# Kernel tuning notes

Hardware: AMD Instinct MI355X
Metric: run time of the kernel (lower is better)

Reference implementation:

```python
import jax, jax.numpy as jnp
import numpy as np

HIDDEN = 1024
N_HEADS = 16
HEAD_DIM = HIDDEN // N_HEADS


def setup_inputs() -> dict:
    key = jax.random.key(0)
    ks = jax.random.split(key, 7)
    b, l, m = 4, 1024, 1024
    q = jax.random.normal(ks[0], (b, l, HIDDEN), dtype=jnp.float32)
    k = jax.random.normal(ks[1], (b, m, HIDDEN), dtype=jnp.float32)
    v = jax.random.normal(ks[2], (b, m, HIDDEN), dtype=jnp.float32)
    s = 1.0 / np.sqrt(HIDDEN)
    w_q = jax.random.normal(ks[3], (HIDDEN, HIDDEN), dtype=jnp.float32) * s
    w_k = jax.random.normal(ks[4], (HIDDEN, HIDDEN), dtype=jnp.float32) * s
    w_v = jax.random.normal(ks[5], (HIDDEN, HIDDEN), dtype=jnp.float32) * s
    w_o = jax.random.normal(ks[6], (HIDDEN, HIDDEN), dtype=jnp.float32) * s
    return {"q": q, "k": k, "v": v, "w_q": w_q, "w_k": w_k, "w_v": w_v, "w_o": w_o}


def reference(q, k, v, w_q, w_k, w_v, w_o):
    b, l, _ = q.shape
    _, m, _ = k.shape
    # Linear (bias=False): y = x @ W^T
    qp = q @ w_q.T
    kp = k @ w_k.T
    vp = v @ w_v.T  # projected but unused downstream (faithful to original bug)
    # Faithful non-standard split: hidden -> (head_dim, n_heads)
    qh = qp.reshape(b, l, HEAD_DIM, N_HEADS)
    kh = kp.reshape(b, m, HEAD_DIM, N_HEADS)
    # attn over K, scaled, softmax over m (dim=2)
    scores = jnp.einsum('bldn,bmdn->blmn', qh, kh) / np.sqrt(HEAD_DIM)
    attn = jax.nn.softmax(scores, axis=2)
    # dropout is identity in eval mode
    # NOTE: original attends over K (not V) — reproduced faithfully
    x = jnp.einsum('blmn,bmdn->bldn', attn, kh)
    x = x.reshape(b, l, HIDDEN)  # 'b l d n -> b l (d n)'
    return x @ w_o.T
```

## Files before the change

kernel.cpp:

```cpp
#include <hip/hip_runtime.h>
#include <hip/hip_bf16.h>
#include <stdint.h>
#include <math.h>


typedef __bf16 bf16;
typedef __bf16 bf16x8 __attribute__((ext_vector_type(8)));
typedef __bf16 bf16x4 __attribute__((ext_vector_type(4)));
typedef float  f32x4  __attribute__((ext_vector_type(4)));
typedef float  f32x16 __attribute__((ext_vector_type(16)));

__device__ __forceinline__ void async_load16(const void* g, void* l) {
  __builtin_amdgcn_global_load_lds((__attribute__((address_space(1))) void*)g,
                                   (__attribute__((address_space(3))) void*)l,
                                   16, 0, 0);
}

__device__ __forceinline__ void join_pin() {
  __builtin_amdgcn_sched_barrier(0);
  __builtin_amdgcn_s_barrier();
  __builtin_amdgcn_sched_barrier(0);
}

__device__ __forceinline__ int detect_fl(const void* samp, int tid, int* smax) {
  int e = (((const unsigned short*)samp)[tid] >> 7) & 0xFF;
#pragma unroll
  for (int off = 1; off <= 32; off <<= 1) {
    int o = __shfl_xor(e, off);
    e = o > e ? o : e;
  }
  if ((tid & 63) == 0) smax[tid >> 6] = e;
  __syncthreads();
  int m01 = smax[0] > smax[1] ? smax[0] : smax[1];
  int m23 = smax[2] > smax[3] ? smax[2] : smax[3];
  return ((m01 > m23 ? m01 : m23) >= 140) ? 1 : 0;
}

__global__ void __launch_bounds__(256)
canon(const void* __restrict__ q, const void* __restrict__ k,
      const void* __restrict__ wq, const void* __restrict__ wk,
      const void* __restrict__ wo,
      bf16* __restrict__ qc, bf16* __restrict__ kc,
      bf16* __restrict__ wqc, bf16* __restrict__ wkc,
      bf16* __restrict__ wo_p, int* __restrict__ flag) {
  __shared__ int smax[4];
  const int tid = threadIdx.x;
  const int fl = detect_fl(q, tid, smax);
  if (blockIdx.x == 0 && tid == 0) *flag = fl;

  const size_t e0 = (size_t)blockIdx.x * 2048 + tid * 8;
  const size_t M4 = 4194304, M8 = 8388608, M9 = 9437184, M10 = 10485760;
  const void* src; bf16* dst; size_t le; bool perm = false;
  if (e0 < M4)       { src = q;  dst = qc;   le = e0;       }
  else if (e0 < M8)  { src = k;  dst = kc;   le = e0 - M4;  }
  else if (e0 < M9)  { src = wq; dst = wqc;  le = e0 - M8;  }
  else if (e0 < M10) { src = wk; dst = wkc;  le = e0 - M9;  }
  else               { src = wo; dst = wo_p; le = e0 - M10; perm = true; }

  if (!perm) {
    bf16x8 v;
    if (fl) {
      const float* p = (const float*)src + le;
      f32x4 a = *(const f32x4*)p, b = *(const f32x4*)(p + 4);
#pragma unroll
      for (int j = 0; j < 4; ++j) { v[j] = (bf16)a[j]; v[4 + j] = (bf16)b[j]; }
    } else {
      v = *(const bf16x8*)((const bf16*)src + le);
    }
    *(bf16x8*)(dst + le) = v;
  } else {
    int o = (int)(le >> 10), kp0 = (int)(le & 1023);
    bf16x8 v;
#pragma unroll
    for (int j = 0; j < 8; ++j) {
      int kp = kp0 + j;
      int h = ((kp & 63) << 4) | (kp >> 6);
      float f = fl ? ((const float*)src)[o * 1024 + h]
                   : (float)((const bf16*)src)[o * 1024 + h];
      f = fminf(fmaxf(f, -1024.f), 1024.f);
      v[j] = (bf16)f;
    }
    *(bf16x8*)(dst + le) = v;
  }
}

__global__ void __launch_bounds__(256, 3)
qk_gemm(const bf16* __restrict__ qc, const bf16* __restrict__ wqc,
        const bf16* __restrict__ kc, const bf16* __restrict__ wkc,
        bf16* __restrict__ qh, bf16* __restrict__ kh, bf16* __restrict__ khT,
        float cs) {
  __shared__ __align__(16) char smem[49152];
  bf16* const sA0 = (bf16*)smem;
  bf16* const sA1 = (bf16*)(smem + 16384);
  bf16* const sB0 = (bf16*)(smem + 32768);
  bf16* const sB1 = (bf16*)(smem + 40960);
  bf16* const epi = (bf16*)smem;

  const int tid  = threadIdx.x;
  const int lane = tid & 63;
  const int wave = tid >> 6;
  const int q4   = lane >> 4;
  const int c16  = lane & 15;
  const int wm   = wave >> 1;
  const int wn   = wave & 1;

  const int z = blockIdx.z;
  const bf16* A = z ? kc : qc;
  const bf16* W = z ? wkc : wqc;
  const float scale = z ? 1.0f : cs;
  bf16* out0 = z ? kh : qh;

  const int lin    = blockIdx.x + 8 * blockIdx.y;
  const int rowBlk = (lin & 31) * 128;
  const int colBlk = (lin >> 5) * 64;

  const bf16* gA[4]; int lA[4];
#pragma unroll
  for (int i = 0; i < 4; ++i) {
    int s = tid + 256 * i;
    int r = s >> 3, g = (s & 7) ^ (r & 7);
    gA[i] = A + (size_t)(rowBlk + r) * 1024 + g * 8;
    lA[i] = s * 8;
  }
  const bf16* gB[2]; int lB[2];
#pragma unroll
  for (int i = 0; i < 2; ++i) {
    int s = tid + 256 * i;
    int r = s >> 3, g = (s & 7) ^ (r & 7);
    gB[i] = W + (size_t)(colBlk + r) * 1024 + g * 8;
    lB[i] = s * 8;
  }

  f32x4 acc[4][2] = {};

#pragma unroll
  for (int i = 0; i < 4; ++i) async_load16(gA[i], sA0 + lA[i]);
#pragma unroll
  for (int i = 0; i < 2; ++i) async_load16(gB[i], sB0 + lB[i]);

  for (int t = 0; t < 16; ++t) {
    if (t < 15) {
      const int kn = (t + 1) * 64;
      bf16* dA = (t & 1) ? sA0 : sA1;
      bf16* dB = (t & 1) ? sB0 : sB1;
#pragma unroll
      for (int i = 0; i < 4; ++i) async_load16(gA[i] + kn, dA + lA[i]);
#pragma unroll
      for (int i = 0; i < 2; ++i) async_load16(gB[i] + kn, dB + lB[i]);
      asm volatile("s_waitcnt vmcnt(6)" ::: "memory");
    } else {
      asm volatile("s_waitcnt vmcnt(0)" ::: "memory");
    }
    join_pin();

    const bf16* cA = (t & 1) ? sA1 : sA0;
    const bf16* cB = (t & 1) ? sB1 : sB0;
#pragma unroll
    for (int ks = 0; ks < 2; ++ks) {
      bf16x8 af[4], bfr[2];
#pragma unroll
      for (int mt = 0; mt < 4; ++mt) {
        int row = wm * 64 + mt * 16 + c16;
        af[mt] = *(const bf16x8*)(cA + row * 64 +
                   (((ks * 4 + q4) ^ (row & 7)) * 8));
      }
#pragma unroll
      for (int nt = 0; nt < 2; ++nt) {
        int row = wn * 32 + nt * 16 + c16;
        bfr[nt] = *(const bf16x8*)(cB + row * 64 +
                   (((ks * 4 + q4) ^ (row & 7)) * 8));
      }
#pragma unroll
      for (int mt = 0; mt < 4; ++mt)
#pragma unroll
        for (int nt = 0; nt < 2; ++nt)
          acc[mt][nt] = __builtin_amdgcn_mfma_f32_16x16x32_bf16(
              af[mt], bfr[nt], acc[mt][nt], 0, 0, 0);
    }
    asm volatile("s_waitcnt lgkmcnt(0)" ::: "memory");
    join_pin();
  }

#pragma unroll
  for (int mt = 0; mt < 4; ++mt)
#pragma unroll
    for (int nt = 0; nt < 2; ++nt)
#pragma unroll
      for (int r = 0; r < 4; ++r) {
        int m_t = wm * 64 + mt * 16 + q4 * 4 + r;
        int c   = wn * 32 + nt * 16 + c16;
        epi[m_t * 70 + c] = (bf16)(acc[mt][nt][r] * scale);
      }
  __syncthreads();

  const int bb    = rowBlk >> 10;
  const int mbase = rowBlk & 1023;
  const int dg0   = colBlk >> 4;

  {
    int n = tid >> 4;
#pragma unroll
    for (int i = 0; i < 8; ++i) {
      int m_t = (tid & 15) + i * 16;
      bf16x4 v;
#pragma unroll
      for (int dt = 0; dt < 4; ++dt) v[dt] = epi[m_t * 70 + dt * 16 + n];
      *(bf16x4*)(out0 + ((size_t)(bb * 16 + n) * 1024 + mbase + m_t) * 64 + dg0) = v;
    }
  }
  if (z) {
    int r = tid >> 2, qtr = tid & 3;
    int n = r >> 2, dt = r & 3;
    int c = dt * 16 + n;
    size_t base = ((size_t)(bb * 16 + n) * 64 + dg0 + dt) * 1024 + mbase + qtr * 32;
#pragma unroll
    for (int c8 = 0; c8 < 4; ++c8) {
      bf16x8 v;
#pragma unroll
      for (int j = 0; j < 8; ++j) v[j] = epi[(qtr * 32 + c8 * 8 + j) * 70 + c];
      *(bf16x8*)(khT + base + c8 * 8) = v;
    }
  }
}

__global__ void __launch_bounds__(256, 2)
attn_kernel(const bf16* __restrict__ qh, const bf16* __restrict__ kh,
            const bf16* __restrict__ khT, bf16* __restrict__ xh) {
  __shared__ __align__(16) bf16 sK[2][64 * 64];
  __shared__ __align__(16) bf16 sKT[2][64 * 64];
  __shared__ __align__(16) bf16 sP[4][32 * 72];

  const int tid  = threadIdx.x;
  const int lane = tid & 63;
  const int wave = tid >> 6;
  const int n32  = lane & 31;
  const int hk   = lane >> 5;
  const int lin  = blockIdx.x;
  const int bn   = lin & 63;
  const int qt   = lin >> 6;
  const int b    = bn >> 4, n = bn & 15;
  const int l0w  = qt * 128 + wave * 32;

  const bf16* qhead  = qh  + (size_t)bn * (1024 * 64);
  const bf16* khead  = kh  + (size_t)bn * (1024 * 64);
  const bf16* kThead = khT + (size_t)bn * (64 * 1024);

  bf16x8 aq[4];
#pragma unroll
  for (int kc = 0; kc < 4; ++kc)
    aq[kc] = *(const bf16x8*)(qhead + (size_t)(l0w + n32) * 64 + kc * 16 + hk * 8);

  int kr[2], kg[2];
#pragma unroll
  for (int i = 0; i < 2; ++i) {
    int s = tid + 256 * i;
    kr[i] = s >> 3;  kg[i] = (s & 7) ^ (kr[i] & 7);
  }

  f32x16 O[2] = {};
  f32x16 Osum = {};
  bf16x8 ones;
#pragma unroll
  for (int j = 0; j < 8; ++j) ones[j] = (bf16)1.0f;
  bf16* sPw = sP[wave];

#pragma unroll
  for (int i = 0; i < 2; ++i) {
    int s = (tid + 256 * i) * 8;
    async_load16(khead + (size_t)kr[i] * 64 + kg[i] * 8, &sK[0][s]);
    async_load16(kThead + (size_t)kr[i] * 1024 + kg[i] * 8, &sKT[0][s]);
  }

  for (int t = 0; t < 16; ++t) {
    if (t < 15) {
      const int m0n = (t + 1) * 64;
      const int bi  = (t + 1) & 1;
#pragma unroll
      for (int i = 0; i < 2; ++i) {
        int s = (tid + 256 * i) * 8;
        async_load16(khead + (size_t)(m0n + kr[i]) * 64 + kg[i] * 8, &sK[bi][s]);
        async_load16(kThead + (size_t)kr[i] * 1024 + m0n + kg[i] * 8, &sKT[bi][s]);
      }
      asm volatile("s_waitcnt vmcnt(4)" ::: "memory");
    } else {
      asm volatile("s_waitcnt vmcnt(0)" ::: "memory");
    }
    join_pin();

    const bf16* cK  = sK[t & 1];
    const bf16* cKT = sKT[t & 1];

    f32x16 S0 = {}, S1 = {};
    __builtin_amdgcn_s_setprio(1);
#pragma unroll
    for (int kc = 0; kc < 4; ++kc) {
      int G = kc * 2 + hk;
      int R0 = n32, R1 = 32 + n32;
      bf16x8 bk0 = *(const bf16x8*)(cK + R0 * 64 + ((G ^ (R0 & 7)) * 8));
      bf16x8 bk1 = *(const bf16x8*)(cK + R1 * 64 + ((G ^ (R1 & 7)) * 8));
      S0 = __builtin_amdgcn_mfma_f32_32x32x16_bf16(aq[kc], bk0, S0, 0, 0, 0);
      S1 = __builtin_amdgcn_mfma_f32_32x32x16_bf16(aq[kc], bk1, S1, 0, 0, 0);
    }
    __builtin_amdgcn_s_setprio(0);

#pragma unroll
    for (int r = 0; r < 16; ++r) {
      int qrow = (r & 3) + 8 * (r >> 2) + 4 * hk;
      sPw[qrow * 72 + n32]      = (bf16)__builtin_amdgcn_exp2f(S0[r]);
      sPw[qrow * 72 + 32 + n32] = (bf16)__builtin_amdgcn_exp2f(S1[r]);
    }

    bf16x8 ap[4];
    __builtin_amdgcn_s_setprio(1);
#pragma unroll
    for (int kc = 0; kc < 4; ++kc) {
      ap[kc] = *(const bf16x8*)(sPw + n32 * 72 + kc * 16 + hk * 8);
      Osum = __builtin_amdgcn_mfma_f32_32x32x16_bf16(ap[kc], ones, Osum, 0, 0, 0);
    }
#pragma unroll
    for (int dt = 0; dt < 2; ++dt) {
#pragma unroll
      for (int kc = 0; kc < 4; ++kc) {
        int R = dt * 32 + n32;
        int G = kc * 2 + hk;
        bf16x8 bkt = *(const bf16x8*)(cKT + R * 64 + ((G ^ (R & 7)) * 8));
        O[dt] = __builtin_amdgcn_mfma_f32_32x32x16_bf16(ap[kc], bkt, O[dt], 0, 0, 0);
      }
    }
    __builtin_amdgcn_s_setprio(0);
    asm volatile("s_waitcnt lgkmcnt(0)" ::: "memory");
    join_pin();
  }

  {
    float inv[16];
#pragma unroll
    for (int r = 0; r < 16; ++r) inv[r] = 1.0f / Osum[r];
#pragma unroll
    for (int dt = 0; dt < 2; ++dt)
#pragma unroll
      for (int r = 0; r < 16; ++r) {
        int qrow = (r & 3) + 8 * (r >> 2) + 4 * hk;
        sPw[qrow * 72 + dt * 32 + n32] = (bf16)(O[dt][r] * inv[r]);
      }
  }
  {
    int l_loc = lane >> 1, dh = lane & 1;
    size_t base = ((size_t)(b * 1024 + l0w + l_loc) * 16 + n) * 64 + dh * 32;
#pragma unroll
    for (int c8 = 0; c8 < 4; ++c8) {
      bf16x8 v = *(const bf16x8*)(sPw + l_loc * 72 + dh * 32 + c8 * 8);
      *(bf16x8*)(xh + base + c8 * 8) = v;
    }
  }
}

__global__ void __launch_bounds__(256, 4)
o_gemm(const bf16* __restrict__ A, const bf16* __restrict__ W,
       bf16* __restrict__ out0, float* __restrict__ outf,
       const int* __restrict__ flag) {
  __shared__ __align__(16) bf16 sA[2][64 * 64];
  __shared__ __align__(16) bf16 sB[2][64 * 64];

  const int tid  = threadIdx.x;
  const int lane = tid & 63;
  const int wave = tid >> 6;
  const int q4   = lane >> 4;
  const int c16  = lane & 15;
  const int wm   = wave >> 1;
  const int wn   = wave & 1;

  const int lin    = blockIdx.x + 8 * blockIdx.y;
  const int rowBlk = (lin & 63) * 64;
  const int colBlk = (lin >> 6) * 64;

  const bf16* gA[2]; const bf16* gB[2]; int ls[2];
#pragma unroll
  for (int i = 0; i < 2; ++i) {
    int s = tid + 256 * i;
    int r = s >> 3, g = (s & 7) ^ (r & 7);
    gA[i] = A + (size_t)(rowBlk + r) * 1024 + g * 8;
    gB[i] = W + (size_t)(colBlk + r) * 1024 + g * 8;
    ls[i] = s * 8;
  }

  f32x4 acc[2][2] = {};

#pragma unroll
  for (int i = 0; i < 2; ++i) {
    async_load16(gA[i], &sA[0][ls[i]]);
    async_load16(gB[i], &sB[0][ls[i]]);
  }

  for (int t = 0; t < 16; ++t) {
    if (t < 15) {
      const int kn = (t + 1) * 64;
      const int bi = (t + 1) & 1;
#pragma unroll
      for (int i = 0; i < 2; ++i) {
        async_load16(gA[i] + kn, &sA[bi][ls[i]]);
        async_load16(gB[i] + kn, &sB[bi][ls[i]]);
      }
      asm volatile("s_waitcnt vmcnt(4)" ::: "memory");
    } else {
      asm volatile("s_waitcnt vmcnt(0)" ::: "memory");
    }
    join_pin();

    const bf16* cA = sA[t & 1];
    const bf16* cB = sB[t & 1];
#pragma unroll
    for (int ks = 0; ks < 2; ++ks) {
      bf16x8 af[2], bfr[2];
#pragma unroll
      for (int mt = 0; mt < 2; ++mt) {
        int row = wm * 32 + mt * 16 + c16;
        af[mt] = *(const bf16x8*)(cA + row * 64 +
                   (((ks * 4 + q4) ^ (row & 7)) * 8));
      }
#pragma unroll
      for (int nt = 0; nt < 2; ++nt) {
        int row = wn * 32 + nt * 16 + c16;
        bfr[nt] = *(const bf16x8*)(cB + row * 64 +
                   (((ks * 4 + q4) ^ (row & 7)) * 8));
      }
#pragma unroll
      for (int mt = 0; mt < 2; ++mt)
#pragma unroll
        for (int nt = 0; nt < 2; ++nt)
          acc[mt][nt] = __builtin_amdgcn_mfma_f32_16x16x32_bf16(
              af[mt], bfr[nt], acc[mt][nt], 0, 0, 0);
    }
    asm volatile("s_waitcnt lgkmcnt(0)" ::: "memory");
    join_pin();
  }

  const int fl = *flag;
#pragma unroll
  for (int mt = 0; mt < 2; ++mt)
#pragma unroll
    for (int nt = 0; nt < 2; ++nt)
#pragma unroll
      for (int r = 0; r < 4; ++r) {
        int gm = rowBlk + wm * 32 + mt * 16 + q4 * 4 + r;
        int gn = colBlk + wn * 32 + nt * 16 + c16;
        size_t idx = (size_t)gm * 1024 + gn;
        if (fl) outf[idx] = acc[mt][nt][r];
        else    out0[idx] = (bf16)acc[mt][nt][r];
      }
}

extern "C" void kernel_launch(void* const* d_in, const int* in_sizes, int n_in,
                              void* d_out, int out_size, void* d_ws, size_t ws_size,
                              hipStream_t stream) {
  const void* q_raw  = d_in[0];
  const void* k_raw  = d_in[1];
  const void* wq_raw = d_in[3];
  const void* wk_raw = d_in[4];
  const void* wo_raw = d_in[6];

  char* ws = (char*)d_ws;
  const size_t MB = 1024 * 1024;
  bf16* qc   = (bf16*)(ws + 0 * MB);
  bf16* kc   = (bf16*)(ws + 8 * MB);
  bf16* kh   = (bf16*)(ws + 16 * MB);
  bf16* wqc  = (bf16*)(ws + 24 * MB);
  bf16* wkc  = (bf16*)(ws + 26 * MB);
  bf16* wo_p = (bf16*)(ws + 28 * MB);
  int*  flag = (int*)(ws + 30 * MB);
  bf16* xh   = qc;
  bf16* qh   = (bf16*)d_out;
  bf16* khT  = (bf16*)((char*)d_out + 8 * MB);

  const float CS = 0.125f * 1.4426950408889634f;
  dim3 blk(256, 1, 1);

  hipLaunchKernelGGL(canon, dim3(5632), blk, 0, stream,
                     q_raw, k_raw, wq_raw, wk_raw, wo_raw,
                     qc, kc, wqc, wkc, wo_p, flag);
  hipLaunchKernelGGL(qk_gemm, dim3(8, 64, 2), blk, 0, stream,
                     qc, wqc, kc, wkc, qh, kh, khT, CS);
  hipLaunchKernelGGL(attn_kernel, dim3(512), blk, 0, stream,
                     qh, kh, khT, xh);
  hipLaunchKernelGGL(o_gemm, dim3(8, 128), blk, 0, stream,
                     xh, wo_p, (bf16*)d_out, (float*)d_out, flag);
}
```

Before: 188.3 us.

## Fuse fp32-to-bf16 activation conversion into the QK projection GEMM loads

The q and k activations are no longer converted to bf16 in a separate pass. The QK GEMM now reads the raw fp32 (or bf16) activations into registers, converts them, and stores them to LDS, prefetching one tile ahead. The canon kernel now handles only the weights. This removes a full read-and-write round trip of 8M activation elements and shrinks the canon launch. In exchange, the GEMM A-side loses its async direct-to-LDS loads, does twice the global bytes per tile in fp32 mode, and adds register pressure, conversion ALU work and an extra LDS wait.

```diff
diff --git a/kernel.cpp b/kernel.cpp
--- a/kernel.cpp
+++ b/kernel.cpp
@@ -37,10 +37,8 @@
 }
 
 __global__ void __launch_bounds__(256)
-canon(const void* __restrict__ q, const void* __restrict__ k,
-      const void* __restrict__ wq, const void* __restrict__ wk,
-      const void* __restrict__ wo,
-      bf16* __restrict__ qc, bf16* __restrict__ kc,
+canon(const void* __restrict__ q, const void* __restrict__ wq,
+      const void* __restrict__ wk, const void* __restrict__ wo,
       bf16* __restrict__ wqc, bf16* __restrict__ wkc,
       bf16* __restrict__ wo_p, int* __restrict__ flag) {
   __shared__ int smax[4];
@@ -49,13 +47,11 @@
   if (blockIdx.x == 0 && tid == 0) *flag = fl;
 
   const size_t e0 = (size_t)blockIdx.x * 2048 + tid * 8;
-  const size_t M4 = 4194304, M8 = 8388608, M9 = 9437184, M10 = 10485760;
+  const size_t M1 = 1048576, M2 = 2097152;
   const void* src; bf16* dst; size_t le; bool perm = false;
-  if (e0 < M4)       { src = q;  dst = qc;   le = e0;       }
-  else if (e0 < M8)  { src = k;  dst = kc;   le = e0 - M4;  }
-  else if (e0 < M9)  { src = wq; dst = wqc;  le = e0 - M8;  }
-  else if (e0 < M10) { src = wk; dst = wkc;  le = e0 - M9;  }
-  else               { src = wo; dst = wo_p; le = e0 - M10; perm = true; }
+  if (e0 < M1)      { src = wq; dst = wqc;  le = e0;      }
+  else if (e0 < M2) { src = wk; dst = wkc;  le = e0 - M1; }
+  else              { src = wo; dst = wo_p; le = e0 - M2; perm = true; }
 
   if (!perm) {
     bf16x8 v;
@@ -85,8 +81,8 @@
 }
 
 __global__ void __launch_bounds__(256, 3)
-qk_gemm(const bf16* __restrict__ qc, const bf16* __restrict__ wqc,
-        const bf16* __restrict__ kc, const bf16* __restrict__ wkc,
+qk_gemm(const void* __restrict__ q_raw, const bf16* __restrict__ wqc,
+        const void* __restrict__ k_raw, const bf16* __restrict__ wkc,
         bf16* __restrict__ qh, bf16* __restrict__ kh, bf16* __restrict__ khT,
         float cs) {
   __shared__ __align__(16) char smem[49152];
@@ -95,6 +91,7 @@
   bf16* const sB0 = (bf16*)(smem + 32768);
   bf16* const sB1 = (bf16*)(smem + 40960);
   bf16* const epi = (bf16*)smem;
+  __shared__ int smax[4];
 
   const int tid  = threadIdx.x;
   const int lane = tid & 63;
@@ -104,9 +101,11 @@
   const int wm   = wave >> 1;
   const int wn   = wave & 1;
 
+  const int fl = detect_fl(q_raw, tid, smax);
+
   const int z = blockIdx.z;
-  const bf16* A = z ? kc : qc;
-  const bf16* W = z ? wkc : wqc;
+  const void* A  = z ? k_raw : q_raw;
+  const bf16* W  = z ? wkc : wqc;
   const float scale = z ? 1.0f : cs;
   bf16* out0 = z ? kh : qh;
 
@@ -114,13 +113,12 @@
   const int rowBlk = (lin & 31) * 128;
   const int colBlk = (lin >> 5) * 64;
 
-  const bf16* gA[4]; int lA[4];
+  size_t aoff[4];
 #pragma unroll
   for (int i = 0; i < 4; ++i) {
     int s = tid + 256 * i;
     int r = s >> 3, g = (s & 7) ^ (r & 7);
-    gA[i] = A + (size_t)(rowBlk + r) * 1024 + g * 8;
-    lA[i] = s * 8;
+    aoff[i] = (size_t)(rowBlk + r) * 1024 + g * 8;
   }
   const bf16* gB[2]; int lB[2];
 #pragma unroll
@@ -132,28 +130,62 @@
   }
 
   f32x4 acc[4][2] = {};
-
-#pragma unroll
-  for (int i = 0; i < 4; ++i) async_load16(gA[i], sA0 + lA[i]);
+  f32x4 pA[4][2];
+  bf16x8 hA[4];
+
+  if (fl) {
+#pragma unroll
+    for (int i = 0; i < 4; ++i) {
+      const float* p = (const float*)A + aoff[i];
+      pA[i][0] = *(const f32x4*)p; pA[i][1] = *(const f32x4*)(p + 4);
+    }
+  } else {
+#pragma unroll
+    for (int i = 0; i < 4; ++i)
+      hA[i] = *(const bf16x8*)((const bf16*)A + aoff[i]);
+  }
 #pragma unroll
   for (int i = 0; i < 2; ++i) async_load16(gB[i], sB0 + lB[i]);
 
   for (int t = 0; t < 16; ++t) {
+    bf16* dA = (t & 1) ? sA1 : sA0;
+    if (fl) {
+#pragma unroll
+      for (int i = 0; i < 4; ++i) {
+        bf16x8 st;
+#pragma unroll
+        for (int j = 0; j < 4; ++j) { st[j] = (bf16)pA[i][0][j]; st[4 + j] = (bf16)pA[i][1][j]; }
+        *(bf16x8*)(dA + (tid + 256 * i) * 8) = st;
+      }
+    } else {
+#pragma unroll
+      for (int i = 0; i < 4; ++i) *(bf16x8*)(dA + (tid + 256 * i) * 8) = hA[i];
+    }
     if (t < 15) {
       const int kn = (t + 1) * 64;
-      bf16* dA = (t & 1) ? sA0 : sA1;
+      if (fl) {
+#pragma unroll
+        for (int i = 0; i < 4; ++i) {
+          const float* p = (const float*)A + aoff[i] + kn;
+          pA[i][0] = *(const f32x4*)p; pA[i][1] = *(const f32x4*)(p + 4);
+        }
+      } else {
+#pragma unroll
+        for (int i = 0; i < 4; ++i)
+          hA[i] = *(const bf16x8*)((const bf16*)A + aoff[i] + kn);
+      }
       bf16* dB = (t & 1) ? sB0 : sB1;
 #pragma unroll
-      for (int i = 0; i < 4; ++i) async_load16(gA[i] + kn, dA + lA[i]);
-#pragma unroll
       for (int i = 0; i < 2; ++i) async_load16(gB[i] + kn, dB + lB[i]);
-      asm volatile("s_waitcnt vmcnt(6)" ::: "memory");
+      if (fl) asm volatile("s_waitcnt vmcnt(10)" ::: "memory");
+      else    asm volatile("s_waitcnt vmcnt(6)"  ::: "memory");
     } else {
       asm volatile("s_waitcnt vmcnt(0)" ::: "memory");
     }
+    asm volatile("s_waitcnt lgkmcnt(0)" ::: "memory");
     join_pin();
 
-    const bf16* cA = (t & 1) ? sA1 : sA0;
+    const bf16* cA = dA;
     const bf16* cB = (t & 1) ? sB1 : sB0;
 #pragma unroll
     for (int ks = 0; ks < 2; ++ks) {
@@ -461,25 +493,23 @@
 
   char* ws = (char*)d_ws;
   const size_t MB = 1024 * 1024;
-  bf16* qc   = (bf16*)(ws + 0 * MB);
-  bf16* kc   = (bf16*)(ws + 8 * MB);
+  bf16* xh   = (bf16*)(ws + 0 * MB);
   bf16* kh   = (bf16*)(ws + 16 * MB);
   bf16* wqc  = (bf16*)(ws + 24 * MB);
   bf16* wkc  = (bf16*)(ws + 26 * MB);
   bf16* wo_p = (bf16*)(ws + 28 * MB);
   int*  flag = (int*)(ws + 30 * MB);
-  bf16* xh   = qc;
   bf16* qh   = (bf16*)d_out;
   bf16* khT  = (bf16*)((char*)d_out + 8 * MB);
 
   const float CS = 0.125f * 1.4426950408889634f;
   dim3 blk(256, 1, 1);
 
-  hipLaunchKernelGGL(canon, dim3(5632), blk, 0, stream,
-                     q_raw, k_raw, wq_raw, wk_raw, wo_raw,
-                     qc, kc, wqc, wkc, wo_p, flag);
+  hipLaunchKernelGGL(canon, dim3(1536), blk, 0, stream,
+                     q_raw, wq_raw, wk_raw, wo_raw,
+                     wqc, wkc, wo_p, flag);
   hipLaunchKernelGGL(qk_gemm, dim3(8, 64, 2), blk, 0, stream,
-                     qc, wqc, kc, wkc, qh, kh, khT, CS);
+                     q_raw, wqc, k_raw, wkc, qh, kh, khT, CS);
   hipLaunchKernelGGL(attn_kernel, dim3(512), blk, 0, stream,
                      qh, kh, khT, xh);
   hipLaunchKernelGGL(o_gemm, dim3(8, 128), blk, 0, stream,
```

Result: slower. 200.5 us (+6.5%).
